# Optimization experiments

Hardware: AMD Instinct MI355X
Metric: run time of the kernel (lower is better)

## Reference

```python
import jax, jax.numpy as jnp
import numpy as np

N = 4096        # nodes
E = 65536       # edges (avg degree 16)
L = 64          # latent_dims
K = 256         # kernel_dims
ED = 6          # edge_dims
DEPTH = 2


def _gelu(x):
    # torch.nn.GELU / F.gelu default = exact erf form
    return jax.nn.gelu(x, approximate=False)


def setup_inputs() -> dict:
    key = jax.random.key(0)
    ks = jax.random.split(key, 12)
    u = lambda k, shape, fan: jax.random.uniform(k, shape, jnp.float32, -1.0, 1.0) / np.sqrt(fan)
    return {
        "nodes": jax.random.normal(ks[0], (N, L), jnp.float32),
        "edge_index": jax.random.randint(ks[1], (2, E), 0, N, jnp.int32),
        "edge_attr": jax.random.uniform(ks[2], (E, ED), jnp.float32),
        # DenseNet kernel MLP: ED -> K -> K -> L*L (GELU between layers)
        "W1": u(ks[3], (ED, K), ED), "b1": jnp.zeros((K,), jnp.float32),
        "W2": u(ks[4], (K, K), K),  "b2": jnp.zeros((K,), jnp.float32),
        "W3": u(ks[5], (K, L * L), K), "b3": jnp.zeros((L * L,), jnp.float32),
        # NNConv root linear (no bias) + conv bias
        "W_root": u(ks[6], (L, L), L),
        "bias": jnp.zeros((L,), jnp.float32),
    }


def reference(nodes, edge_index, edge_attr, W1, b1, W2, b2, W3, b3, W_root, bias):
    src, dst = edge_index[0], edge_index[1]
    # Edge-conditioned dynamic weights (depend only on edge_attr -> compute once)
    h = _gelu(edge_attr @ W1 + b1)          # [E, K]
    h = _gelu(h @ W2 + b2)                  # [E, K]
    W_edge = (h @ W3 + b3).reshape(E, L, L) # [E, L_in, L_out]

    def conv(x):
        msg = jnp.einsum('ei,eio->eo', x[src], W_edge)          # gather + per-edge matmul
        agg = jax.ops.segment_sum(msg, dst, num_segments=N)     # scatter-add to dst
        return agg + x @ W_root + bias

    x = nodes
    for idx in range(DEPTH):
        x = conv(x)
        if idx < DEPTH - 1:
            x = _gelu(x)
    return x
```

## Files before the change

kernel.cpp:

```cpp
#include <hip/hip_runtime.h>
#include <math.h>

#define NN 4096
#define NE 65536
#define LL 64
#define KK 256
#define ED 6
#define MAXSUPER 6144

typedef __bf16 bf16_t;
typedef __attribute__((ext_vector_type(4))) __bf16 bf16x4;
typedef __attribute__((ext_vector_type(8))) __bf16 bf16x8;
typedef __attribute__((ext_vector_type(4))) float f32x4;
typedef __attribute__((ext_vector_type(16))) float f32x16;

#define OFF_CNT    ((size_t)0)
#define OFF_DESC   ((size_t)16384)
#define OFF_AGG0   ((size_t)147456)
#define OFF_AGG1   ((size_t)1196032)
#define ZERO_BYTES ((size_t)2244608)
#define OFF_CURSOR ((size_t)2244608)
#define OFF_SORTED ((size_t)2260992)
#define OFF_W2R    ((size_t)2785280)
#define OFF_W3RR   ((size_t)2916352)
#define OFF_Q0     ((size_t)5013504)
#define OFF_Q1     ((size_t)6062080)
#define OFF_X1F    ((size_t)7110656)
#define OFF_X0BF   ((size_t)8159232)
#define OFF_X1BF   ((size_t)8683520)
#define OFF_H      ((size_t)9207808)
#define OFF_P      ((size_t)42762240)

__device__ __forceinline__ float gelu_f(float x) {
    return 0.5f * x * (1.0f + erff(x * 0.7071067811865476f));
}
__device__ __forceinline__ bf16_t f2bf(float x) { return (bf16_t)x; }

__global__ void k_hist(const int* __restrict__ ei, int* __restrict__ cnt) {
    int e = blockIdx.x * 256 + threadIdx.x;
    atomicAdd(&cnt[ei[e]], 1);
}

__global__ void k_scan(const int* __restrict__ cnt, int* __restrict__ cursor,
                       int4* __restrict__ descs) {
    __shared__ int pd[1024], pc[1024];
    int t = threadIdx.x;
    int deg[4]; int sd = 0, sc = 0;
#pragma unroll
    for (int j = 0; j < 4; j++) {
        deg[j] = cnt[t * 4 + j];
        sd += deg[j];
        sc += (deg[j] + 31) >> 5;
    }
    pd[t] = sd; pc[t] = sc;
    __syncthreads();
    for (int off = 1; off < 1024; off <<= 1) {
        int vd = 0, vc = 0;
        if (t >= off) { vd = pd[t - off]; vc = pc[t - off]; }
        __syncthreads();
        pd[t] += vd; pc[t] += vc;
        __syncthreads();
    }
    int rd = (t > 0) ? pd[t - 1] : 0;
    int rc = (t > 0) ? pc[t - 1] : 0;
    for (int j = 0; j < 4; j++) {
        int v = t * 4 + j, d = deg[j];
        cursor[v] = rd;
        int nch = (d + 31) >> 5;
        for (int c = 0; c < nch; c++) {
            int rem = d - c * 32;
            descs[rc + c] = make_int4(v, rd + c * 32, rem < 32 ? rem : 32, 0);
        }
        rc += nch; rd += d;
    }
}

__global__ void __launch_bounds__(256) k_fuse3(
        const int* __restrict__ ei, int* __restrict__ cursor, int2* __restrict__ sorted,
        const float* __restrict__ W3, bf16_t* __restrict__ W3rr,
        const float* __restrict__ W2, bf16_t* __restrict__ W2r,
        const float* __restrict__ attr, const float* __restrict__ W1,
        const float* __restrict__ b1, bf16_t* __restrict__ a1,
        const float* __restrict__ x, const float* __restrict__ b3,
        bf16_t* __restrict__ xbf, float* __restrict__ Q) {
    __shared__ float smem[4096];
    int bid = blockIdx.x, tid = threadIdx.x;
    if (bid < 256) {
        int e = bid * 256 + tid;
        int s = ei[e], d = ei[NE + e];
        int pos = atomicAdd(&cursor[s], 1);
        sorted[pos] = make_int2(e, d);
    } else if (bid < 512) {
        int k0 = bid - 256;
        for (int idx = tid; idx < 4096; idx += 256)
            smem[idx] = W3[(size_t)k0 * 4096 + idx];
        __syncthreads();
        int sbase = (2 * (k0 >> 4)) * 512 + (((k0 >> 3) & 1) * 32) * 8 + (k0 & 7);
#pragma unroll
        for (int m = 0; m < 2; m++) {
            int w = m * 256 + tid;
            int o = w >> 3, ib = w & 7;
            int s = sbase + (o >> 5) * 512 + (o & 31) * 8;
            int f = (s >> 4) * 1024 + (ib >> 2) * 512 + (ib & 3) * 128 + (s & 15) * 8;
            bf16x8 pk;
#pragma unroll
            for (int j = 0; j < 8; j++) pk[j] = f2bf(smem[(ib * 8 + j) * 64 + o]);
            *(bf16x8*)(W3rr + f) = pk;
        }
    } else if (bid < 768) {
        int t = (bid - 512) * 256 + tid;
        int kk = t >> 13, nn = (t >> 9) & 15, lane = (t >> 3) & 63, j = t & 7;
        int k = kk * 32 + (lane >> 4) * 8 + j;
        int n = nn * 16 + (lane & 15);
        W2r[t] = f2bf(W2[k * 256 + n]);
    } else if (bid < 1792) {
        float* sa = smem;
        int e0 = (bid - 768) * 64;
        for (int i = tid; i < 64 * ED; i += 256) sa[i] = attr[(size_t)e0 * ED + i];
        int col4 = (tid & 63) * 4;
        float w[ED][4], bb[4];
#pragma unroll
        for (int j = 0; j < ED; j++)
#pragma unroll
            for (int c = 0; c < 4; c++) w[j][c] = W1[j * 256 + col4 + c];
#pragma unroll
        for (int c = 0; c < 4; c++) bb[c] = b1[col4 + c];
        __syncthreads();
        int esub = tid >> 6;
#pragma unroll 1
        for (int eg = 0; eg < 16; eg++) {
            int el = eg * 4 + esub;
            float av[ED];
#pragma unroll
            for (int j = 0; j < ED; j++) av[j] = sa[el * ED + j];
            bf16x4 ov;
#pragma unroll
            for (int c = 0; c < 4; c++) {
                float acc = bb[c];
#pragma unroll
                for (int j = 0; j < ED; j++) acc += av[j] * w[j][c];
                ov[c] = f2bf(gelu_f(acc));
            }
            *(bf16x4*)(a1 + (size_t)(e0 + el) * 256 + col4) = ov;
        }
    } else {
        int v = (bid - 1792) * 4 + (tid >> 6);
        int o = tid & 63;
        float xv = x[v * 64 + o];
        smem[tid] = xv;
        xbf[v * 64 + o] = f2bf(xv);
        __syncthreads();
        const float* sx = smem + (tid >> 6) * 64;
        float q = 0.0f;
#pragma unroll 8
        for (int i = 0; i < 64; i++) q += sx[i] * b3[i * 64 + o];
        Q[v * 64 + o] = q;
    }
}

__device__ __forceinline__ void pgemm_body(const bf16_t* __restrict__ xbf,
                                           const bf16_t* __restrict__ W3rr,
                                           bf16_t* __restrict__ P,
                                           bf16_t* __restrict__ sw_wave,
                                           int strip, int rg) {
    int wave = threadIdx.x >> 6, lane = threadIdx.x & 63;
    int col = lane & 15, quad = lane >> 4;
    int half = lane >> 5, l5 = lane & 31;
    bf16_t* sw = sw_wave + wave * 4224;
    bf16x8 b[16][2];
#pragma unroll
    for (int nn = 0; nn < 16; nn++) {
        int sn = strip * 16 + nn;
#pragma unroll
        for (int ki = 0; ki < 2; ki++)
            b[nn][ki] = *(const bf16x8*)(W3rr + (size_t)(sn * 2 + ki) * 512 + lane * 8);
    }
#pragma unroll 1
    for (int rt = 0; rt < 4; rt++) {
        int rowbase = rg * 256 + wave * 64 + rt * 16;
        const bf16_t* arow = xbf + (size_t)(rowbase + col) * 64;
        bf16x8 a0 = *(const bf16x8*)(arow + quad * 8);
        bf16x8 a1v = *(const bf16x8*)(arow + 32 + quad * 8);
#pragma unroll
        for (int nn = 0; nn < 16; nn++) {
            f32x4 acc;
#pragma unroll
            for (int r = 0; r < 4; r++) acc[r] = 0.0f;
            acc = __builtin_amdgcn_mfma_f32_16x16x32_bf16(b[nn][0], a0, acc, 0, 0, 0);
            acc = __builtin_amdgcn_mfma_f32_16x16x32_bf16(b[nn][1], a1v, acc, 0, 0, 0);
            bf16x4 pk;
#pragma unroll
            for (int r = 0; r < 4; r++) pk[r] = f2bf(acc[r]);
            *(bf16x4*)(sw + col * 264 + nn * 16 + quad * 4) = pk;
        }
        __builtin_amdgcn_wave_barrier();
#pragma unroll
        for (int i = 0; i < 8; i++) {
            int r2 = 2 * i + half;
            bf16x8 vb = *(const bf16x8*)(sw + r2 * 264 + l5 * 8);
            *(bf16x8*)(P + (size_t)(rowbase + r2) * 16384 + strip * 256 + l5 * 8) = vb;
        }
        __builtin_amdgcn_wave_barrier();
    }
}

__global__ void __launch_bounds__(256) k_fuse4(const bf16_t* __restrict__ xbf,
                                               const bf16_t* __restrict__ W3rr,
                                               bf16_t* __restrict__ P,
                                               const bf16_t* __restrict__ a1,
                                               const bf16_t* __restrict__ W2r,
                                               const float* __restrict__ b2,
                                               bf16_t* __restrict__ h) {
    __shared__ bf16_t sB[16896];
    if (blockIdx.x < 1024) {
        pgemm_body(xbf, W3rr, P, sB, blockIdx.x & 63, blockIdx.x >> 6);
    } else {
        int tid = threadIdx.x;
        int wave = tid >> 6, lane = tid & 63, col = lane & 15, quad = lane >> 4;
        int base = (blockIdx.x - 1024) * 128 + wave * 32;
        bf16x8 a[2][8];
#pragma unroll
        for (int t = 0; t < 2; t++) {
            const bf16_t* arow = a1 + (size_t)(base + t * 16 + col) * 256;
#pragma unroll
            for (int kk = 0; kk < 8; kk++)
                a[t][kk] = *(const bf16x8*)(arow + kk * 32 + quad * 8);
        }
#pragma unroll 1
        for (int p = 0; p < 4; p++) {
#pragma unroll
            for (int it = 0; it < 8; it++) {
                int c = it * 256 + tid;
                int fl = c >> 6;
                int e = (c & 63) * 8;
                int kk = fl >> 2, nnl = fl & 3;
                *(bf16x8*)(sB + fl * 512 + e) =
                    *(const bf16x8*)(W2r + (size_t)(kk * 16 + p * 4 + nnl) * 512 + e);
            }
            __syncthreads();
#pragma unroll
            for (int nnl = 0; nnl < 4; nnl++) {
                f32x4 acc0, acc1;
#pragma unroll
                for (int r = 0; r < 4; r++) { acc0[r] = 0.0f; acc1[r] = 0.0f; }
#pragma unroll
                for (int kk = 0; kk < 8; kk++) {
                    bf16x8 b = *(const bf16x8*)(sB + (kk * 4 + nnl) * 512 + lane * 8);
                    acc0 = __builtin_amdgcn_mfma_f32_16x16x32_bf16(a[0][kk], b, acc0, 0, 0, 0);
                    acc1 = __builtin_amdgcn_mfma_f32_16x16x32_bf16(a[1][kk], b, acc1, 0, 0, 0);
                }
                int ncol = (p * 4 + nnl) * 16 + col;
                float bv = b2[ncol];
#pragma unroll
                for (int r = 0; r < 4; r++) {
                    int row0 = base + quad * 4 + r;
                    h[(size_t)row0 * 256 + ncol] = f2bf(gelu_f(acc0[r] + bv));
                    h[(size_t)(row0 + 16) * 256 + ncol] = f2bf(gelu_f(acc1[r] + bv));
                }
            }
            __syncthreads();
        }
    }
}

__global__ void __launch_bounds__(256) k_pgemm(const bf16_t* __restrict__ xbf,
                                               const bf16_t* __restrict__ W3rr,
                                               bf16_t* __restrict__ P) {
    __shared__ bf16_t sw_all[16896];
    pgemm_body(xbf, W3rr, P, sw_all, blockIdx.x & 63, blockIdx.x >> 6);
}

__global__ void __launch_bounds__(256) k_agg(const int4* __restrict__ descs,
                                             const int2* __restrict__ sorted,
                                             const bf16_t* __restrict__ h,
                                             const bf16_t* __restrict__ P,
                                             const float* __restrict__ Q,
                                             float* __restrict__ agg) {
    int chunk = blockIdx.x * 4 + (threadIdx.x >> 6);
    int lane = threadIdx.x & 63;
    int row = lane & 31, khalf = lane >> 5;
    int4 d = descs[chunk];
    int v = d.x, base = d.y, cnt = d.z;
    if (cnt == 0) return;
    bool valid = (row < cnt);
    int2 ed = sorted[base + (valid ? row : 0)];
    int eid = ed.x, dst = ed.y;

    bf16x8 zero;
#pragma unroll
    for (int i = 0; i < 8; i++) zero[i] = (bf16_t)0.0f;

    bf16x8 a[16];
    const bf16_t* hrow = h + (size_t)eid * 256;
#pragma unroll
    for (int kt = 0; kt < 16; kt++) {
        bf16x8 t = *(const bf16x8*)(hrow + kt * 16 + khalf * 8);
        a[kt] = valid ? t : zero;
    }
    const bf16_t* Pv = P + (size_t)v * 16384;
    f32x16 acc0, acc1;
#pragma unroll
    for (int r = 0; r < 16; r++) { acc0[r] = 0.0f; acc1[r] = 0.0f; }
#pragma unroll
    for (int kt = 0; kt < 16; kt++) {
        bf16x8 b0 = *(const bf16x8*)(Pv + (size_t)(kt * 2 + 0) * 512 + lane * 8);
        bf16x8 b1 = *(const bf16x8*)(Pv + (size_t)(kt * 2 + 1) * 512 + lane * 8);
        acc0 = __builtin_amdgcn_mfma_f32_32x32x16_bf16(a[kt], b0, acc0, 0, 0, 0);
        acc1 = __builtin_amdgcn_mfma_f32_32x32x16_bf16(a[kt], b1, acc1, 0, 0, 0);
    }
    float q0 = Q[v * 64 + row];
    float q1 = Q[v * 64 + 32 + row];
#pragma unroll
    for (int r = 0; r < 16; r++) {
        int mm = (r & 3) + 8 * (r >> 2) + 4 * khalf;
        int de = __shfl(dst, mm, 64);
        if (mm < cnt) {
            atomicAdd(&agg[(size_t)de * 64 + row], acc0[r] + q0);
            atomicAdd(&agg[(size_t)de * 64 + 32 + row], acc1[r] + q1);
        }
    }
}

__global__ void k_combine1(const float* __restrict__ x, const float* __restrict__ agg,
                           const float* __restrict__ Wroot, const float* __restrict__ bias,
                           const float* __restrict__ b3, float* __restrict__ x1,
                           bf16_t* __restrict__ x1bf, float* __restrict__ Q1) {
    __shared__ float sx[64], sy[64];
    int v = blockIdx.x, o = threadIdx.x;
    sx[o] = x[v * 64 + o];
    __syncthreads();
    float acc = agg[v * 64 + o] + bias[o];
#pragma unroll 8
    for (int i = 0; i < 64; i++) acc += sx[i] * Wroot[i * 64 + o];
    acc = gelu_f(acc);
    x1[v * 64 + o] = acc;
    x1bf[v * 64 + o] = f2bf(acc);
    sy[o] = acc;
    __syncthreads();
    float q = 0.0f;
#pragma unroll 8
    for (int i = 0; i < 64; i++) q += sy[i] * b3[i * 64 + o];
    Q1[v * 64 + o] = q;
}

__global__ void k_combine2(const float* __restrict__ x1, const float* __restrict__ agg,
                           const float* __restrict__ Wroot, const float* __restrict__ bias,
                           float* __restrict__ out) {
    __shared__ float sx[64];
    int v = blockIdx.x, o = threadIdx.x;
    sx[o] = x1[v * 64 + o];
    __syncthreads();
    float acc = agg[v * 64 + o] + bias[o];
#pragma unroll 8
    for (int i = 0; i < 64; i++) acc += sx[i] * Wroot[i * 64 + o];
    out[v * 64 + o] = acc;
}

extern "C" void kernel_launch(void* const* d_in, const int* in_sizes, int n_in,
                              void* d_out, int out_size, void* d_ws, size_t ws_size,
                              hipStream_t stream) {
    const float* nodes = (const float*)d_in[0];
    const int*   ei    = (const int*)d_in[1];
    const float* attr  = (const float*)d_in[2];
    const float* W1    = (const float*)d_in[3];
    const float* b1    = (const float*)d_in[4];
    const float* W2    = (const float*)d_in[5];
    const float* b2    = (const float*)d_in[6];
    const float* W3    = (const float*)d_in[7];
    const float* b3    = (const float*)d_in[8];
    const float* Wroot = (const float*)d_in[9];
    const float* bias  = (const float*)d_in[10];
    float* out = (float*)d_out;
    char* ws = (char*)d_ws;

    int*    cnt    = (int*)(ws + OFF_CNT);
    int4*   descs  = (int4*)(ws + OFF_DESC);
    float*  agg0   = (float*)(ws + OFF_AGG0);
    float*  agg1   = (float*)(ws + OFF_AGG1);
    int*    cursor = (int*)(ws + OFF_CURSOR);
    int2*   sorted = (int2*)(ws + OFF_SORTED);
    bf16_t* W2r    = (bf16_t*)(ws + OFF_W2R);
    bf16_t* W3rr   = (bf16_t*)(ws + OFF_W3RR);
    float*  Q0     = (float*)(ws + OFF_Q0);
    float*  Q1     = (float*)(ws + OFF_Q1);
    float*  x1f    = (float*)(ws + OFF_X1F);
    bf16_t* x0bf   = (bf16_t*)(ws + OFF_X0BF);
    bf16_t* x1bf   = (bf16_t*)(ws + OFF_X1BF);
    bf16_t* hbuf   = (bf16_t*)(ws + OFF_H);
    bf16_t* a1buf  = (bf16_t*)(ws + OFF_H);
    bf16_t* Pbuf   = (bf16_t*)(ws + OFF_P);

    hipMemsetAsync(ws, 0, ZERO_BYTES, stream);
    k_hist<<<NE / 256, 256, 0, stream>>>(ei, cnt);
    k_scan<<<1, 1024, 0, stream>>>(cnt, cursor, descs);
    k_fuse3<<<2816, 256, 0, stream>>>(ei, cursor, sorted, W3, W3rr, W2, W2r,
                                      attr, W1, b1, a1buf, nodes, b3, x0bf, Q0);
    k_fuse4<<<1536, 256, 0, stream>>>(x0bf, W3rr, Pbuf, a1buf, W2r, b2, hbuf);
    k_agg<<<MAXSUPER / 4, 256, 0, stream>>>(descs, sorted, hbuf, Pbuf, Q0, agg0);
    k_combine1<<<NN, 64, 0, stream>>>(nodes, agg0, Wroot, bias, b3, x1f, x1bf, Q1);
    k_pgemm<<<1024, 256, 0, stream>>>(x1bf, W3rr, Pbuf);
    k_agg<<<MAXSUPER / 4, 256, 0, stream>>>(descs, sorted, hbuf, Pbuf, Q1, agg1);
    k_combine2<<<NN, 64, 0, stream>>>(x1f, agg1, Wroot, bias, out);
}
```

Measured before the change: 267.4 us.

## Stage W3 strip in shared memory and write P via block-wide transpose tiles

The P-GEMM body now cooperatively loads the whole W3 strip into LDS once per block instead of holding 32 bf16x8 B-fragments in registers per wave. Each wave now handles a 16-row slice of a 64-row block, and outputs are staged through a shared 64x128 transpose buffer in two phases. Stores to P are then written as wider contiguous row segments across the block. This is meant to cut register pressure and improve store coalescing, at the cost of more LDS traffic, block-level barriers, and higher LDS usage per block.

New measurement: 278.7 us. +4.2%, slower.

```diff
diff --git a/kernel.cpp b/kernel.cpp
--- a/kernel.cpp
+++ b/kernel.cpp
@@ -161,46 +161,54 @@
 __device__ __forceinline__ void pgemm_body(const bf16_t* __restrict__ xbf,
                                            const bf16_t* __restrict__ W3rr,
                                            bf16_t* __restrict__ P,
-                                           bf16_t* __restrict__ sw_wave,
+                                           bf16_t* __restrict__ sW,
+                                           bf16_t* __restrict__ sT,
                                            int strip, int rg) {
-    int wave = threadIdx.x >> 6, lane = threadIdx.x & 63;
+    int tid = threadIdx.x;
+    int wave = tid >> 6, lane = tid & 63;
     int col = lane & 15, quad = lane >> 4;
-    int half = lane >> 5, l5 = lane & 31;
-    bf16_t* sw = sw_wave + wave * 4224;
-    bf16x8 b[16][2];
-#pragma unroll
-    for (int nn = 0; nn < 16; nn++) {
-        int sn = strip * 16 + nn;
-#pragma unroll
-        for (int ki = 0; ki < 2; ki++)
-            b[nn][ki] = *(const bf16x8*)(W3rr + (size_t)(sn * 2 + ki) * 512 + lane * 8);
-    }
+    const bf16x8* gsrc = (const bf16x8*)(W3rr + (size_t)strip * 16384);
+    bf16x8* ldst = (bf16x8*)sW;
+#pragma unroll
+    for (int it = 0; it < 8; it++)
+        ldst[it * 256 + tid] = gsrc[it * 256 + tid];
+    __syncthreads();
 #pragma unroll 1
     for (int rt = 0; rt < 4; rt++) {
-        int rowbase = rg * 256 + wave * 64 + rt * 16;
+        int rowblk = rg * 256 + rt * 64;
+        int rowbase = rowblk + wave * 16;
         const bf16_t* arow = xbf + (size_t)(rowbase + col) * 64;
         bf16x8 a0 = *(const bf16x8*)(arow + quad * 8);
         bf16x8 a1v = *(const bf16x8*)(arow + 32 + quad * 8);
-#pragma unroll
-        for (int nn = 0; nn < 16; nn++) {
-            f32x4 acc;
-#pragma unroll
-            for (int r = 0; r < 4; r++) acc[r] = 0.0f;
-            acc = __builtin_amdgcn_mfma_f32_16x16x32_bf16(b[nn][0], a0, acc, 0, 0, 0);
-            acc = __builtin_amdgcn_mfma_f32_16x16x32_bf16(b[nn][1], a1v, acc, 0, 0, 0);
-            bf16x4 pk;
-#pragma unroll
-            for (int r = 0; r < 4; r++) pk[r] = f2bf(acc[r]);
-            *(bf16x4*)(sw + col * 264 + nn * 16 + quad * 4) = pk;
-        }
-        __builtin_amdgcn_wave_barrier();
-#pragma unroll
-        for (int i = 0; i < 8; i++) {
-            int r2 = 2 * i + half;
-            bf16x8 vb = *(const bf16x8*)(sw + r2 * 264 + l5 * 8);
-            *(bf16x8*)(P + (size_t)(rowbase + r2) * 16384 + strip * 256 + l5 * 8) = vb;
-        }
-        __builtin_amdgcn_wave_barrier();
+#pragma unroll 1
+        for (int phase = 0; phase < 2; phase++) {
+#pragma unroll
+            for (int nn = 0; nn < 8; nn++) {
+                int fn = phase * 8 + nn;
+                bf16x8 b0 = *(const bf16x8*)(sW + (fn * 2 + 0) * 512 + lane * 8);
+                bf16x8 b1 = *(const bf16x8*)(sW + (fn * 2 + 1) * 512 + lane * 8);
+                f32x4 acc;
+#pragma unroll
+                for (int r = 0; r < 4; r++) acc[r] = 0.0f;
+                acc = __builtin_amdgcn_mfma_f32_16x16x32_bf16(b0, a0, acc, 0, 0, 0);
+                acc = __builtin_amdgcn_mfma_f32_16x16x32_bf16(b1, a1v, acc, 0, 0, 0);
+                bf16x4 pk;
+#pragma unroll
+                for (int r = 0; r < 4; r++) pk[r] = f2bf(acc[r]);
+                *(bf16x4*)(sT + (wave * 16 + col) * 132 + nn * 16 + quad * 4) = pk;
+            }
+            __syncthreads();
+#pragma unroll
+            for (int it = 0; it < 4; it++) {
+                int c = it * 256 + tid;
+                int row = c >> 4;
+                int cp = (c & 15) * 8;
+                bf16x8 vd = *(const bf16x8*)(sT + row * 132 + cp);
+                *(bf16x8*)(P + (size_t)(rowblk + row) * 16384 +
+                           strip * 256 + phase * 128 + cp) = vd;
+            }
+            __syncthreads();
+        }
     }
 }
 
@@ -211,9 +219,10 @@
                                                const bf16_t* __restrict__ W2r,
                                                const float* __restrict__ b2,
                                                bf16_t* __restrict__ h) {
-    __shared__ bf16_t sB[16896];
+    __shared__ bf16_t sW[16384];
+    __shared__ bf16_t sT[8448];
     if (blockIdx.x < 1024) {
-        pgemm_body(xbf, W3rr, P, sB, blockIdx.x & 63, blockIdx.x >> 6);
+        pgemm_body(xbf, W3rr, P, sW, sT, blockIdx.x & 63, blockIdx.x >> 6);
     } else {
         int tid = threadIdx.x;
         int wave = tid >> 6, lane = tid & 63, col = lane & 15, quad = lane >> 4;
@@ -234,7 +243,7 @@
                 int fl = c >> 6;
                 int e = (c & 63) * 8;
                 int kk = fl >> 2, nnl = fl & 3;
-                *(bf16x8*)(sB + fl * 512 + e) =
+                *(bf16x8*)(sW + fl * 512 + e) =
                     *(const bf16x8*)(W2r + (size_t)(kk * 16 + p * 4 + nnl) * 512 + e);
             }
             __syncthreads();
@@ -245,7 +254,7 @@
                 for (int r = 0; r < 4; r++) { acc0[r] = 0.0f; acc1[r] = 0.0f; }
 #pragma unroll
                 for (int kk = 0; kk < 8; kk++) {
-                    bf16x8 b = *(const bf16x8*)(sB + (kk * 4 + nnl) * 512 + lane * 8);
+                    bf16x8 b = *(const bf16x8*)(sW + (kk * 4 + nnl) * 512 + lane * 8);
                     acc0 = __builtin_amdgcn_mfma_f32_16x16x32_bf16(a[0][kk], b, acc0, 0, 0, 0);
                     acc1 = __builtin_amdgcn_mfma_f32_16x16x32_bf16(a[1][kk], b, acc1, 0, 0, 0);
                 }
@@ -266,8 +275,9 @@
 __global__ void __launch_bounds__(256) k_pgemm(const bf16_t* __restrict__ xbf,
                                                const bf16_t* __restrict__ W3rr,
                                                bf16_t* __restrict__ P) {
-    __shared__ bf16_t sw_all[16896];
-    pgemm_body(xbf, W3rr, P, sw_all, blockIdx.x & 63, blockIdx.x >> 6);
+    __shared__ bf16_t sW[16384];
+    __shared__ bf16_t sT[8448];
+    pgemm_body(xbf, W3rr, P, sW, sT, blockIdx.x & 63, blockIdx.x >> 6);
 }
 
 __global__ void __launch_bounds__(256) k_agg(const int4* __restrict__ descs,
```
